# Kernel tuning notes

Measured on AMD Instinct MI355X. Metric: run time of the kernel, lower is better.

The kernel has to match this reference:

```python
import jax, jax.numpy as jnp
import numpy as np

BN_EPS = 1e-5

def _ste_sign(x):
    # forward: sign in {-1,+1}; backward: clipped straight-through (grad 1 on [-1,1])
    s = jnp.where(x >= 0, 1.0, -1.0).astype(x.dtype)
    c = jnp.clip(x, -1.0, 1.0)
    return c + jax.lax.stop_gradient(s - c)

def setup_inputs() -> dict:
    key = jax.random.key(0)
    ks = jax.random.split(key, 8)
    N, C, H, W = 32, 256, 56, 56
    x = jax.random.normal(ks[0], (N, C, H, W), dtype=jnp.float32)
    bias0 = jax.random.normal(ks[1], (C,), dtype=jnp.float32) * 0.1
    w = jax.random.normal(ks[2], (C, C, 1, 1), dtype=jnp.float32) * 0.05
    gamma = jnp.ones((C,), dtype=jnp.float32)
    beta = jnp.zeros((C,), dtype=jnp.float32)
    bias1 = jax.random.normal(ks[3], (C,), dtype=jnp.float32) * 0.1
    alpha = jnp.full((C,), 0.25, dtype=jnp.float32)  # PReLU init
    bias2 = jax.random.normal(ks[4], (C,), dtype=jnp.float32) * 0.1
    return {"x": x, "bias0": bias0, "w": w, "gamma": gamma, "beta": beta,
            "bias1": bias1, "alpha": alpha, "bias2": bias2}

def reference(x, bias0, w, gamma, beta, bias1, alpha, bias2):
    ch = lambda v: v[None, :, None, None]
    # move0: learnable per-channel bias
    out = x + ch(bias0)
    # binary activation: sign (STE)
    out = _ste_sign(out)
    # binarized 1x1 conv: w_bin = mean(|w|) per out-channel * sign(w)
    scale = jnp.mean(jnp.abs(w), axis=(1, 2, 3))              # [O]
    wb = scale[:, None] * _ste_sign(w[:, :, 0, 0])            # [O, C]
    out = jnp.einsum('nchw,oc->nohw', out, wb)                # 1x1 conv
    # bn1: batch statistics (training-mode math)
    mu = jnp.mean(out, axis=(0, 2, 3), keepdims=True)
    var = jnp.var(out, axis=(0, 2, 3), keepdims=True)
    out = ch(gamma) * (out - mu) * jax.lax.rsqrt(var + BN_EPS) + ch(beta)
    # residual add (downsample is None)
    out = out + x
    # move1 -> PReLU -> move2
    out = out + ch(bias1)
    out = jnp.where(out > 0, out, ch(alpha) * out)
    out = out + ch(bias2)
    return out
```

## Files before the change

kernel.cpp:

```cpp
#include <hip/hip_runtime.h>
#include <stdint.h>

typedef unsigned long long u64;
typedef unsigned int u32;
typedef float f32x4 __attribute__((ext_vector_type(4)));

constexpr int kC  = 256;
constexpr int kHW = 3136;
constexpr int kN  = 32;
constexpr int kP  = kN * kHW;
constexpr int kTile = 256;
constexpr int kBlkT = kP / kTile;
constexpr int kRedBlk  = 8;
constexpr int kRedRows = kBlkT / kRedBlk;

constexpr size_t OFF_T     = 0;
constexpr size_t OFF_SCALE = 8192;
constexpr size_t OFF_SUMD  = 9216;
constexpr size_t OFF_SUMD2 = 11264;
constexpr size_t OFF_S     = 13312;
constexpr size_t OFF_PS    = 3224576;
constexpr size_t OFF_PQ    = 4830208;

struct alignas(16) U64x2 { u64 x, y; };

__global__ __launch_bounds__(256) void prep_kernel(
    const float* __restrict__ w, char* __restrict__ ws) {
  int t = threadIdx.x;
  int b = blockIdx.x;
  u64*   T     = (u64*)(ws + OFF_T);
  float* scale = (float*)(ws + OFF_SCALE);
  int kk = t >> 6, ln = t & 63;
  if (b == 0) {
    ((u64*)(ws + OFF_SUMD))[t]  = 0ull;
    ((u64*)(ws + OFF_SUMD2))[t] = 0ull;
  }
  __shared__ float part[4][16];
#pragma unroll
  for (int i = 0; i < 16; ++i) {
    int o = b * 16 + i;
    float v = w[o * kC + kk * 64 + ln];
    u64 m = __ballot(v >= 0.0f);
    float a = fabsf(v);
#pragma unroll
    for (int s = 32; s > 0; s >>= 1) a += __shfl_xor(a, s, 64);
    if (ln == 0) { T[kk * 256 + o] = m; part[kk][i] = a; }
  }
  __syncthreads();
  if (t < 16) {
    int o = b * 16 + t;
    scale[o] = (part[0][t] + part[1][t] + part[2][t] + part[3][t]) * (1.0f / 256.0f);
  }
}

__global__ __launch_bounds__(256) void pack_kernel(
    const float* __restrict__ x, const float* __restrict__ bias0,
    char* __restrict__ ws) {
  int t = threadIdx.x;
  int k    = __builtin_amdgcn_readfirstlane(t >> 6);
  int lane = t & 63;
  u32 p0 = (u32)blockIdx.x * (u32)kTile + 4u * (u32)lane;
  u32 n  = p0 / kHW;
  u32 hw = p0 - n * kHW;
  const float* xp = x + (size_t)(n * kC + k * 64) * kHW + hw;
  const float* bp = bias0 + k * 64;

  u64 m0 = 0, m1 = 0, m2 = 0, m3 = 0;
#pragma unroll 8
  for (int i = 0; i < 64; ++i) {
    f32x4 v = *(const f32x4*)(xp + (size_t)i * kHW);
    float bc = bp[i];
    m0 |= (u64)(v.x + bc >= 0.0f) << i;
    m1 |= (u64)(v.y + bc >= 0.0f) << i;
    m2 |= (u64)(v.z + bc >= 0.0f) << i;
    m3 |= (u64)(v.w + bc >= 0.0f) << i;
  }
  u64* Sp = (u64*)(ws + OFF_S) + (size_t)k * kP + p0;
  U64x2 a; a.x = m0; a.y = m1;
  U64x2 b; b.x = m2; b.y = m3;
  *(U64x2*)Sp       = a;
  *(U64x2*)(Sp + 2) = b;
}

__global__ __launch_bounds__(256) void stats_kernel(char* __restrict__ ws) {
  __shared__ u64 tile[4][kTile];
  int t = threadIdx.x;
  u32 pb = blockIdx.x * (u32)kTile;
  const u64* S = (const u64*)(ws + OFF_S);
#pragma unroll
  for (int q = 0; q < 4; ++q) tile[q][t] = S[(size_t)q * kP + pb + t];

  const u64* T = (const u64*)(ws + OFF_T);
  u64 t0 = T[t], t1 = T[256 + t], t2 = T[512 + t], t3 = T[768 + t];
  __syncthreads();

  int summ = 0, summ2 = 0;
#pragma unroll 4
  for (int j = 0; j < kTile; ++j) {
    int kx = __popcll(tile[0][j] ^ t0) + __popcll(tile[1][j] ^ t1) +
             __popcll(tile[2][j] ^ t2) + __popcll(tile[3][j] ^ t3);
    int mm = 128 - kx;
    summ  += mm;
    summ2 += mm * mm;
  }
  ((int*)(ws + OFF_PS))[blockIdx.x * 256 + t] = summ;
  ((int*)(ws + OFF_PQ))[blockIdx.x * 256 + t] = summ2;
}

__global__ __launch_bounds__(256) void reduce_kernel(char* __restrict__ ws) {
  int t = threadIdx.x;
  int b = blockIdx.x;
  const int* PS = (const int*)(ws + OFF_PS);
  const int* PQ = (const int*)(ws + OFF_PQ);
  long long s = 0, q = 0;
#pragma unroll 7
  for (int r = 0; r < kRedRows; ++r) {
    int row = b * kRedRows + r;
    s += PS[row * 256 + t];
    q += PQ[row * 256 + t];
  }
  atomicAdd((u64*)(ws + OFF_SUMD) + t,  (u64)(long long)(2 * s));
  atomicAdd((u64*)(ws + OFF_SUMD2) + t, (u64)(long long)(4 * q));
}

__global__ __launch_bounds__(256) void finalize_kernel(
    const float* __restrict__ x, const float* __restrict__ gamma,
    const float* __restrict__ beta, const float* __restrict__ bias1,
    const float* __restrict__ alpha, const float* __restrict__ bias2,
    const char* __restrict__ ws, float* __restrict__ out) {
  __shared__ u64   ldsT[256][4];
  __shared__ f32x4 ldsC[256];

  int t = threadIdx.x;
  {
    const u64* T = (const u64*)(ws + OFF_T);
#pragma unroll
    for (int q = 0; q < 4; ++q) ldsT[t][q] = T[q * 256 + t];

    const float*     scale = (const float*)(ws + OFF_SCALE);
    const long long* sumd  = (const long long*)(ws + OFF_SUMD);
    const long long* sumd2 = (const long long*)(ws + OFF_SUMD2);
    double inv  = 1.0 / (double)kP;
    double md   = (double)sumd[t] * inv;
    double e2   = (double)sumd2[t] * inv;
    double vard = e2 - md * md;
    float sc  = scale[t];
    float mu  = sc * (float)md;
    float var = sc * sc * (float)vard;
    float rs  = rsqrtf(var + 1e-5f);
    float g   = gamma[t];
    float cA  = g * rs * sc;
    float cB  = beta[t] - g * rs * mu + bias1[t];
    f32x4 cc; cc.x = 2.0f * cA; cc.y = cB; cc.z = alpha[t]; cc.w = bias2[t];
    ldsC[t] = cc;
  }
  __syncthreads();

  int k    = __builtin_amdgcn_readfirstlane(t >> 6);
  int lane = t & 63;
  u32 p0 = (u32)blockIdx.x * (u32)kTile + 4u * (u32)lane;
  u32 n  = p0 / kHW;
  u32 hw = p0 - n * kHW;

  const u64* S = (const u64*)(ws + OFF_S);
  U64x2 a0 = *(const U64x2*)&S[p0],          b0 = *(const U64x2*)&S[p0 + 2];
  U64x2 a1 = *(const U64x2*)&S[kP + p0],     b1 = *(const U64x2*)&S[kP + p0 + 2];
  U64x2 a2 = *(const U64x2*)&S[2 * kP + p0], b2 = *(const U64x2*)&S[2 * kP + p0 + 2];
  U64x2 a3 = *(const U64x2*)&S[3 * kP + p0], b3 = *(const U64x2*)&S[3 * kP + p0 + 2];

  const float* xp = x   + (size_t)(n * kC + k * 64) * kHW + hw;
  float*       op = out + (size_t)(n * kC + k * 64) * kHW + hw;

#pragma unroll 4
  for (int i = 0; i < 64; ++i) {
    int o = k * 64 + i;
    u64 w0 = ldsT[o][0], w1 = ldsT[o][1], w2 = ldsT[o][2], w3 = ldsT[o][3];
    f32x4 cc = ldsC[o];
    f32x4 xv = *(const f32x4*)(xp + (size_t)i * kHW);
    int k0 = __popcll(a0.x ^ w0) + __popcll(a1.x ^ w1) +
             __popcll(a2.x ^ w2) + __popcll(a3.x ^ w3);
    int k1 = __popcll(a0.y ^ w0) + __popcll(a1.y ^ w1) +
             __popcll(a2.y ^ w2) + __popcll(a3.y ^ w3);
    int k2 = __popcll(b0.x ^ w0) + __popcll(b1.x ^ w1) +
             __popcll(b2.x ^ w2) + __popcll(b3.x ^ w3);
    int k3 = __popcll(b0.y ^ w0) + __popcll(b1.y ^ w1) +
             __popcll(b2.y ^ w2) + __popcll(b3.y ^ w3);
    float u0 = fmaf(cc.x, (float)(128 - k0), cc.y) + xv.x;
    float u1 = fmaf(cc.x, (float)(128 - k1), cc.y) + xv.y;
    float u2 = fmaf(cc.x, (float)(128 - k2), cc.y) + xv.z;
    float u3 = fmaf(cc.x, (float)(128 - k3), cc.y) + xv.w;
    f32x4 r;
    r.x = (u0 > 0.0f ? u0 : cc.z * u0) + cc.w;
    r.y = (u1 > 0.0f ? u1 : cc.z * u1) + cc.w;
    r.z = (u2 > 0.0f ? u2 : cc.z * u2) + cc.w;
    r.w = (u3 > 0.0f ? u3 : cc.z * u3) + cc.w;
    __builtin_nontemporal_store(r, (f32x4*)(op + (size_t)i * kHW));
  }
}

extern "C" void kernel_launch(void* const* d_in, const int* in_sizes, int n_in,
                              void* d_out, int out_size, void* d_ws, size_t ws_size,
                              hipStream_t stream) {
  const float* x     = (const float*)d_in[0];
  const float* bias0 = (const float*)d_in[1];
  const float* w     = (const float*)d_in[2];
  const float* gamma = (const float*)d_in[3];
  const float* beta  = (const float*)d_in[4];
  const float* bias1 = (const float*)d_in[5];
  const float* alpha = (const float*)d_in[6];
  const float* bias2 = (const float*)d_in[7];
  float* out = (float*)d_out;
  char*  ws  = (char*)d_ws;

  hipLaunchKernelGGL(prep_kernel, dim3(16), dim3(256), 0, stream, w, ws);
  hipLaunchKernelGGL(pack_kernel, dim3(kBlkT), dim3(256), 0, stream,
                     x, bias0, ws);
  hipLaunchKernelGGL(stats_kernel, dim3(kBlkT), dim3(256), 0, stream, ws);
  hipLaunchKernelGGL(reduce_kernel, dim3(kRedBlk), dim3(256), 0, stream, ws);
  hipLaunchKernelGGL(finalize_kernel, dim3(kBlkT), dim3(256), 0, stream,
                     x, gamma, beta, bias1, alpha, bias2, ws, out);
}
```

Measured before the change: 255.7 us.

## Fuse sign packing with XNOR-popcount and store per-position counts for finalize

The packing kernel now also computes the binary conv popcounts for its 128 positions, writes the per-output-channel partial sums via wave shuffles, and stores a packed 16-bit count pair per channel/position in a workspace D buffer. This removes the separate stats kernel and the finalize-side recomputation of popcounts. A small coef kernel precomputes the BN/PReLU coefficients once instead of in every finalize block. In exchange the D buffer (about 51 MB) is written and then read back, adding memory traffic. The per-channel shuffle reductions also add work inside the fused kernel.

```diff
diff --git a/kernel.cpp b/kernel.cpp
--- a/kernel.cpp
+++ b/kernel.cpp
@@ -3,24 +3,26 @@
 
 typedef unsigned long long u64;
 typedef unsigned int u32;
+typedef float f32x2 __attribute__((ext_vector_type(2)));
 typedef float f32x4 __attribute__((ext_vector_type(4)));
 
 constexpr int kC  = 256;
 constexpr int kHW = 3136;
 constexpr int kN  = 32;
 constexpr int kP  = kN * kHW;
-constexpr int kTile = 256;
-constexpr int kBlkT = kP / kTile;
-constexpr int kRedBlk  = 8;
-constexpr int kRedRows = kBlkT / kRedBlk;
+constexpr int kPos = 128;
+constexpr int kBlk = kP / kPos;
+constexpr int kRedBlk  = 16;
+constexpr int kRedRows = kBlk / kRedBlk;
 
 constexpr size_t OFF_T     = 0;
 constexpr size_t OFF_SCALE = 8192;
 constexpr size_t OFF_SUMD  = 9216;
 constexpr size_t OFF_SUMD2 = 11264;
-constexpr size_t OFF_S     = 13312;
-constexpr size_t OFF_PS    = 3224576;
-constexpr size_t OFF_PQ    = 4830208;
+constexpr size_t OFF_CC    = 13312;
+constexpr size_t OFF_PS    = 17408;
+constexpr size_t OFF_PQ    = 820224;
+constexpr size_t OFF_D     = 1623040;
 
 struct alignas(16) U64x2 { u64 x, y; };
 
@@ -28,7 +30,7 @@
     const float* __restrict__ w, char* __restrict__ ws) {
   int t = threadIdx.x;
   int b = blockIdx.x;
-  u64*   T     = (u64*)(ws + OFF_T);
+  u64*   T4    = (u64*)(ws + OFF_T);
   float* scale = (float*)(ws + OFF_SCALE);
   int kk = t >> 6, ln = t & 63;
   if (b == 0) {
@@ -44,7 +46,7 @@
     float a = fabsf(v);
 #pragma unroll
     for (int s = 32; s > 0; s >>= 1) a += __shfl_xor(a, s, 64);
-    if (ln == 0) { T[kk * 256 + o] = m; part[kk][i] = a; }
+    if (ln == 0) { T4[o * 4 + kk] = m; part[kk][i] = a; }
   }
   __syncthreads();
   if (t < 16) {
@@ -53,58 +55,59 @@
   }
 }
 
-__global__ __launch_bounds__(256) void pack_kernel(
+__global__ __launch_bounds__(256) void pack_d_kernel(
     const float* __restrict__ x, const float* __restrict__ bias0,
     char* __restrict__ ws) {
+  __shared__ U64x2 tile[4][64];
   int t = threadIdx.x;
   int k    = __builtin_amdgcn_readfirstlane(t >> 6);
   int lane = t & 63;
-  u32 p0 = (u32)blockIdx.x * (u32)kTile + 4u * (u32)lane;
+  u32 pb = (u32)blockIdx.x * (u32)kPos;
+  u32 p0 = pb + 2u * (u32)lane;
   u32 n  = p0 / kHW;
   u32 hw = p0 - n * kHW;
   const float* xp = x + (size_t)(n * kC + k * 64) * kHW + hw;
   const float* bp = bias0 + k * 64;
 
-  u64 m0 = 0, m1 = 0, m2 = 0, m3 = 0;
+  u64 m0 = 0, m1 = 0;
 #pragma unroll 8
   for (int i = 0; i < 64; ++i) {
-    f32x4 v = *(const f32x4*)(xp + (size_t)i * kHW);
+    f32x2 v = *(const f32x2*)(xp + (size_t)i * kHW);
     float bc = bp[i];
     m0 |= (u64)(v.x + bc >= 0.0f) << i;
     m1 |= (u64)(v.y + bc >= 0.0f) << i;
-    m2 |= (u64)(v.z + bc >= 0.0f) << i;
-    m3 |= (u64)(v.w + bc >= 0.0f) << i;
-  }
-  u64* Sp = (u64*)(ws + OFF_S) + (size_t)k * kP + p0;
-  U64x2 a; a.x = m0; a.y = m1;
-  U64x2 b; b.x = m2; b.y = m3;
-  *(U64x2*)Sp       = a;
-  *(U64x2*)(Sp + 2) = b;
-}
-
-__global__ __launch_bounds__(256) void stats_kernel(char* __restrict__ ws) {
-  __shared__ u64 tile[4][kTile];
-  int t = threadIdx.x;
-  u32 pb = blockIdx.x * (u32)kTile;
-  const u64* S = (const u64*)(ws + OFF_S);
+  }
+  U64x2 mm; mm.x = m0; mm.y = m1;
+  tile[k][lane] = mm;
+  __syncthreads();
+
+  U64x2 sa = tile[0][lane], sb = tile[1][lane],
+        sc = tile[2][lane], sd = tile[3][lane];
+
+  const u64* T4 = (const u64*)(ws + OFF_T);
+  u32* D = (u32*)(ws + OFF_D);
+  int myPS = 0, myPQ = 0;
+#pragma unroll 4
+  for (int i = 0; i < 64; ++i) {
+    int o = k * 64 + i;
+    u64 t0 = T4[4 * o], t1 = T4[4 * o + 1], t2 = T4[4 * o + 2], t3 = T4[4 * o + 3];
+    int q0 = __popcll(sa.x ^ t0) + __popcll(sb.x ^ t1) +
+             __popcll(sc.x ^ t2) + __popcll(sd.x ^ t3);
+    int q1 = __popcll(sa.y ^ t0) + __popcll(sb.y ^ t1) +
+             __popcll(sc.y ^ t2) + __popcll(sd.y ^ t3);
+    D[(size_t)o * (kP / 2) + (pb >> 1) + lane] = (u32)q0 | ((u32)q1 << 16);
+    int a0 = 128 - q0, a1 = 128 - q1;
+    int s  = a0 + a1;
+    int sq = a0 * a0 + a1 * a1;
 #pragma unroll
-  for (int q = 0; q < 4; ++q) tile[q][t] = S[(size_t)q * kP + pb + t];
-
-  const u64* T = (const u64*)(ws + OFF_T);
-  u64 t0 = T[t], t1 = T[256 + t], t2 = T[512 + t], t3 = T[768 + t];
-  __syncthreads();
-
-  int summ = 0, summ2 = 0;
-#pragma unroll 4
-  for (int j = 0; j < kTile; ++j) {
-    int kx = __popcll(tile[0][j] ^ t0) + __popcll(tile[1][j] ^ t1) +
-             __popcll(tile[2][j] ^ t2) + __popcll(tile[3][j] ^ t3);
-    int mm = 128 - kx;
-    summ  += mm;
-    summ2 += mm * mm;
-  }
-  ((int*)(ws + OFF_PS))[blockIdx.x * 256 + t] = summ;
-  ((int*)(ws + OFF_PQ))[blockIdx.x * 256 + t] = summ2;
+    for (int msk = 1; msk < 64; msk <<= 1) {
+      s  += __shfl_xor(s,  msk, 64);
+      sq += __shfl_xor(sq, msk, 64);
+    }
+    if (lane == i) { myPS = s; myPQ = sq; }
+  }
+  ((int*)(ws + OFF_PS))[blockIdx.x * 256 + t] = myPS;
+  ((int*)(ws + OFF_PQ))[blockIdx.x * 256 + t] = myPQ;
 }
 
 __global__ __launch_bounds__(256) void reduce_kernel(char* __restrict__ ws) {
@@ -123,78 +126,58 @@
   atomicAdd((u64*)(ws + OFF_SUMD2) + t, (u64)(long long)(4 * q));
 }
 
+__global__ __launch_bounds__(256) void coef_kernel(
+    const float* __restrict__ gamma, const float* __restrict__ beta,
+    const float* __restrict__ bias1, const float* __restrict__ alpha,
+    const float* __restrict__ bias2, char* __restrict__ ws) {
+  int t = threadIdx.x;
+  const float*     scale = (const float*)(ws + OFF_SCALE);
+  const long long* sumd  = (const long long*)(ws + OFF_SUMD);
+  const long long* sumd2 = (const long long*)(ws + OFF_SUMD2);
+  double inv  = 1.0 / (double)kP;
+  double md   = (double)sumd[t] * inv;
+  double e2   = (double)sumd2[t] * inv;
+  double vard = e2 - md * md;
+  float sc  = scale[t];
+  float mu  = sc * (float)md;
+  float var = sc * sc * (float)vard;
+  float rs  = rsqrtf(var + 1e-5f);
+  float g   = gamma[t];
+  float cA  = g * rs * sc;
+  float cB  = beta[t] - g * rs * mu + bias1[t];
+  f32x4 cc; cc.x = 2.0f * cA; cc.y = cB; cc.z = alpha[t]; cc.w = bias2[t];
+  ((f32x4*)(ws + OFF_CC))[t] = cc;
+}
+
 __global__ __launch_bounds__(256) void finalize_kernel(
-    const float* __restrict__ x, const float* __restrict__ gamma,
-    const float* __restrict__ beta, const float* __restrict__ bias1,
-    const float* __restrict__ alpha, const float* __restrict__ bias2,
-    const char* __restrict__ ws, float* __restrict__ out) {
-  __shared__ u64   ldsT[256][4];
-  __shared__ f32x4 ldsC[256];
-
-  int t = threadIdx.x;
-  {
-    const u64* T = (const u64*)(ws + OFF_T);
-#pragma unroll
-    for (int q = 0; q < 4; ++q) ldsT[t][q] = T[q * 256 + t];
-
-    const float*     scale = (const float*)(ws + OFF_SCALE);
-    const long long* sumd  = (const long long*)(ws + OFF_SUMD);
-    const long long* sumd2 = (const long long*)(ws + OFF_SUMD2);
-    double inv  = 1.0 / (double)kP;
-    double md   = (double)sumd[t] * inv;
-    double e2   = (double)sumd2[t] * inv;
-    double vard = e2 - md * md;
-    float sc  = scale[t];
-    float mu  = sc * (float)md;
-    float var = sc * sc * (float)vard;
-    float rs  = rsqrtf(var + 1e-5f);
-    float g   = gamma[t];
-    float cA  = g * rs * sc;
-    float cB  = beta[t] - g * rs * mu + bias1[t];
-    f32x4 cc; cc.x = 2.0f * cA; cc.y = cB; cc.z = alpha[t]; cc.w = bias2[t];
-    ldsC[t] = cc;
-  }
-  __syncthreads();
-
+    const float* __restrict__ x, const char* __restrict__ ws,
+    float* __restrict__ out) {
+  int t = threadIdx.x;
   int k    = __builtin_amdgcn_readfirstlane(t >> 6);
   int lane = t & 63;
-  u32 p0 = (u32)blockIdx.x * (u32)kTile + 4u * (u32)lane;
+  u32 pb = (u32)blockIdx.x * (u32)kPos;
+  u32 p0 = pb + 2u * (u32)lane;
   u32 n  = p0 / kHW;
   u32 hw = p0 - n * kHW;
 
-  const u64* S = (const u64*)(ws + OFF_S);
-  U64x2 a0 = *(const U64x2*)&S[p0],          b0 = *(const U64x2*)&S[p0 + 2];
-  U64x2 a1 = *(const U64x2*)&S[kP + p0],     b1 = *(const U64x2*)&S[kP + p0 + 2];
-  U64x2 a2 = *(const U64x2*)&S[2 * kP + p0], b2 = *(const U64x2*)&S[2 * kP + p0 + 2];
-  U64x2 a3 = *(const U64x2*)&S[3 * kP + p0], b3 = *(const U64x2*)&S[3 * kP + p0 + 2];
-
   const float* xp = x   + (size_t)(n * kC + k * 64) * kHW + hw;
   float*       op = out + (size_t)(n * kC + k * 64) * kHW + hw;
+  const u32*   D  = (const u32*)(ws + OFF_D);
+  const f32x4* CC = (const f32x4*)(ws + OFF_CC);
+  u32 dbase = (pb >> 1) + (u32)lane;
 
 #pragma unroll 4
   for (int i = 0; i < 64; ++i) {
     int o = k * 64 + i;
-    u64 w0 = ldsT[o][0], w1 = ldsT[o][1], w2 = ldsT[o][2], w3 = ldsT[o][3];
-    f32x4 cc = ldsC[o];
-    f32x4 xv = *(const f32x4*)(xp + (size_t)i * kHW);
-    int k0 = __popcll(a0.x ^ w0) + __popcll(a1.x ^ w1) +
-             __popcll(a2.x ^ w2) + __popcll(a3.x ^ w3);
-    int k1 = __popcll(a0.y ^ w0) + __popcll(a1.y ^ w1) +
-             __popcll(a2.y ^ w2) + __popcll(a3.y ^ w3);
-    int k2 = __popcll(b0.x ^ w0) + __popcll(b1.x ^ w1) +
-             __popcll(b2.x ^ w2) + __popcll(b3.x ^ w3);
-    int k3 = __popcll(b0.y ^ w0) + __popcll(b1.y ^ w1) +
-             __popcll(b2.y ^ w2) + __popcll(b3.y ^ w3);
-    float u0 = fmaf(cc.x, (float)(128 - k0), cc.y) + xv.x;
-    float u1 = fmaf(cc.x, (float)(128 - k1), cc.y) + xv.y;
-    float u2 = fmaf(cc.x, (float)(128 - k2), cc.y) + xv.z;
-    float u3 = fmaf(cc.x, (float)(128 - k3), cc.y) + xv.w;
-    f32x4 r;
+    f32x4 cc = CC[o];
+    u32 d = D[(size_t)o * (kP / 2) + dbase];
+    f32x2 xv = *(const f32x2*)(xp + (size_t)i * kHW);
+    float u0 = fmaf(cc.x, (float)(128 - (int)(d & 0xFFFFu)), cc.y) + xv.x;
+    float u1 = fmaf(cc.x, (float)(128 - (int)(d >> 16)),     cc.y) + xv.y;
+    f32x2 r;
     r.x = (u0 > 0.0f ? u0 : cc.z * u0) + cc.w;
     r.y = (u1 > 0.0f ? u1 : cc.z * u1) + cc.w;
-    r.z = (u2 > 0.0f ? u2 : cc.z * u2) + cc.w;
-    r.w = (u3 > 0.0f ? u3 : cc.z * u3) + cc.w;
-    __builtin_nontemporal_store(r, (f32x4*)(op + (size_t)i * kHW));
+    __builtin_nontemporal_store(r, (f32x2*)(op + (size_t)i * kHW));
   }
 }
 
@@ -213,10 +196,11 @@
   char*  ws  = (char*)d_ws;
 
   hipLaunchKernelGGL(prep_kernel, dim3(16), dim3(256), 0, stream, w, ws);
-  hipLaunchKernelGGL(pack_kernel, dim3(kBlkT), dim3(256), 0, stream,
+  hipLaunchKernelGGL(pack_d_kernel, dim3(kBlk), dim3(256), 0, stream,
                      x, bias0, ws);
-  hipLaunchKernelGGL(stats_kernel, dim3(kBlkT), dim3(256), 0, stream, ws);
   hipLaunchKernelGGL(reduce_kernel, dim3(kRedBlk), dim3(256), 0, stream, ws);
-  hipLaunchKernelGGL(finalize_kernel, dim3(kBlkT), dim3(256), 0, stream,
-                     x, gamma, beta, bias1, alpha, bias2, ws, out);
-}
+  hipLaunchKernelGGL(coef_kernel, dim3(1), dim3(256), 0, stream,
+                     gamma, beta, bias1, alpha, bias2, ws);
+  hipLaunchKernelGGL(finalize_kernel, dim3(kBlk), dim3(256), 0, stream,
+                     x, ws, out);
+}
```

After: 273.4 us. 1.07x slower.
